# Optimization experiments

Measured on AMD Instinct MI355X. Metric: run time of the kernel, lower is better.

## Reference

```python
import jax, jax.numpy as jnp
import numpy as np

RESO = (128, 128, 128)      # links table resolution
CAP = 1_600_000             # number of occupied voxels (rows in data arrays)
SH_C = 27                   # 3 * basis_dim (basis_dim = 9 SH components)
N_PTS = 2_000_000           # query points (ray samples)
EMPTY_FRAC = 0.24           # fraction of links marked empty (-1)


def setup_inputs() -> dict:
    key = jax.random.key(0)
    k1, k2, k3, k4, k5 = jax.random.split(key, 5)
    density_data = jax.random.normal(k1, (CAP, 1), dtype=jnp.float32)
    sh_data = 0.1 * jax.random.normal(k2, (CAP, SH_C), dtype=jnp.float32)
    links = jax.random.randint(k3, RESO, 0, CAP, dtype=jnp.int32)
    empty = jax.random.uniform(k4, RESO) < EMPTY_FRAC
    links = jnp.where(empty, jnp.int32(-1), links)
    # points in grid coordinates, spanning the full grid
    points = jax.random.uniform(k5, (N_PTS, 3), dtype=jnp.float32,
                                minval=0.0, maxval=float(RESO[0] - 1))
    return {"density_data": density_data, "sh_data": sh_data,
            "links": links, "points": points}


def reference(density_data, sh_data, links, points):
    """Faithful JAX version of _C.sample_grid (want_colors=True):
    trilinear interpolation of sparse voxel data, where voxel -> data-row
    indirection goes through `links` and negative links contribute zero.
    Returns (out_density [N,1], out_sh [N, 27])."""
    reso = jnp.asarray(links.shape, dtype=points.dtype)
    p = jnp.clip(points, 0.0, reso - 1.0)
    l = jnp.clip(jnp.floor(p).astype(jnp.int32), 0,
                 jnp.asarray(links.shape, jnp.int32) - 2)   # [N,3]
    w = p - l.astype(points.dtype)                           # [N,3] in [0,1]

    out_d = jnp.zeros((points.shape[0], density_data.shape[1]), points.dtype)
    out_sh = jnp.zeros((points.shape[0], sh_data.shape[1]), points.dtype)
    # small fixed loop over 8 corners keeps peak memory at O(N * C)
    for dx in (0, 1):
        wx = w[:, 0] if dx else (1.0 - w[:, 0])
        for dy in (0, 1):
            wy = w[:, 1] if dy else (1.0 - w[:, 1])
            for dz in (0, 1):
                wz = w[:, 2] if dz else (1.0 - w[:, 2])
                idx = links[l[:, 0] + dx, l[:, 1] + dy, l[:, 2] + dz]  # [N]
                valid = idx >= 0
                safe = jnp.where(valid, idx, 0)
                wt = (wx * wy * wz * valid.astype(points.dtype))[:, None]
                out_d = out_d + wt * density_data[safe]
                out_sh = out_sh + wt * sh_data[safe]
    return out_d, out_sh
```

## Files before the change

### kernel.cpp

```cpp
#include <hip/hip_runtime.h>
#include <hip/hip_fp16.h>
#include <hip/hip_fp8.h>

#define RESO 128
#define SH_C 27
#define NCELLS (16*16*16)
#define CAPB 608
#define OVF_CAP 16384
#define PACK_ROWS 64
#define PACK_PER_G 16
#define SCAT_PER_G 5
#define GROUP (PACK_PER_G + SCAT_PER_G)
#define OVF_BLOCKS 64
#define NROWS 729
#define QSTEP 1024.0f
#define QINV  (1.0f/1024.0f)

__device__ __forceinline__ void point_to_voxel(float px, float py, float pz,
                                               int& lx, int& ly, int& lz,
                                               float& cx, float& cy, float& cz) {
    cx = fminf(fmaxf(px, 0.0f), (float)(RESO - 1));
    cy = fminf(fmaxf(py, 0.0f), (float)(RESO - 1));
    cz = fminf(fmaxf(pz, 0.0f), (float)(RESO - 1));
    lx = min(max((int)floorf(cx), 0), RESO - 2);
    ly = min(max((int)floorf(cy), 0), RESO - 2);
    lz = min(max((int)floorf(cz), 0), RESO - 2);
}

__device__ __forceinline__ int cell_of(int lx, int ly, int lz) {
    return ((lx >> 3) << 8) | ((ly >> 3) << 4) | (lz >> 3);
}

#if defined(__has_builtin)
#if __has_builtin(__builtin_amdgcn_cvt_pk_f32_fp8)
#define HAVE_CVT_PK_FP8 1
#endif
#endif

typedef float v2f __attribute__((ext_vector_type(2)));

__device__ __forceinline__ float fp8_to_f32_sw(unsigned int b) {
    const unsigned int s = (b >> 7) & 1u, e = (b >> 3) & 15u, m = b & 7u;
    float v;
    if (e == 0) v = (float)m * 0.001953125f;
    else        v = __uint_as_float(((e + 120u) << 23) | (m << 20));
    return s ? -v : v;
}

__device__ __forceinline__ void acc4_fp8(unsigned int w, float wt, float* a) {
#ifdef HAVE_CVT_PK_FP8
    const v2f lo = __builtin_amdgcn_cvt_pk_f32_fp8((int)w, false);
    const v2f hi = __builtin_amdgcn_cvt_pk_f32_fp8((int)w, true);
    a[0] = fmaf(wt, lo.x, a[0]);
    a[1] = fmaf(wt, lo.y, a[1]);
    a[2] = fmaf(wt, hi.x, a[2]);
    a[3] = fmaf(wt, hi.y, a[3]);
#else
    a[0] = fmaf(wt, fp8_to_f32_sw(w & 0xff), a[0]);
    a[1] = fmaf(wt, fp8_to_f32_sw((w >> 8) & 0xff), a[1]);
    a[2] = fmaf(wt, fp8_to_f32_sw((w >> 16) & 0xff), a[2]);
    a[3] = fmaf(wt, fp8_to_f32_sw((w >> 24) & 0xff), a[3]);
#endif
}

__device__ __forceinline__ void accum_row(const uint4& q0, const uint4& q1,
                                          float wt, float& accd, float* accs) {
    accd = fmaf(wt, __uint_as_float(q0.x), accd);
    acc4_fp8(q0.y, wt, accs + 0);
    acc4_fp8(q0.z, wt, accs + 4);
    acc4_fp8(q0.w, wt, accs + 8);
    acc4_fp8(q1.x, wt, accs + 12);
    acc4_fp8(q1.y, wt, accs + 16);
    acc4_fp8(q1.z, wt, accs + 20);
    acc4_fp8(q1.w, wt, accs + 24);
}

__device__ __forceinline__ void write_out(int orig, float accd, const float* accs,
                                          float* __restrict__ out_d,
                                          float* __restrict__ out_sh) {
    out_d[orig] = accd;
    float* __restrict__ o = out_sh + (size_t)orig * SH_C;
    #pragma unroll
    for (int c = 0; c < SH_C; ++c) o[c] = accs[c];
}

__global__ __launch_bounds__(256) void fused_pack_scatter_kernel(
    const float* __restrict__ density, const float* __restrict__ sh,
    uint4* __restrict__ rows, int cap, int gridp,
    const float* __restrict__ pts, int n, int grids,
    int* __restrict__ cnt, int* __restrict__ ovfcnt,
    uint2* __restrict__ bucket, int* __restrict__ ovf)
{
    __shared__ float sv[PACK_ROWS * SH_C];

    const int bid = blockIdx.x;
    const int g = bid / GROUP, rr = bid % GROUP;

    if (rr < PACK_PER_G) {
        const int pid = g * PACK_PER_G + rr;
        if (pid >= gridp) return;
        const int r0 = pid * PACK_ROWS;
        const int nrows = min(PACK_ROWS, cap - r0);
        if (nrows <= 0) return;
        const float* __restrict__ src = sh + (size_t)r0 * SH_C;
        if (nrows == PACK_ROWS) {
            const float4* __restrict__ s4 = (const float4*)src;
            float4* d4 = (float4*)sv;
            for (int k = threadIdx.x; k < PACK_ROWS * SH_C / 4; k += 256) d4[k] = s4[k];
        } else {
            for (int k = threadIdx.x; k < nrows * SH_C; k += 256) sv[k] = src[k];
        }
        __syncthreads();
        const int t   = threadIdx.x;
        const int row = t >> 2;
        const int s   = t & 3;
        if (row < nrows) {
            const int r = r0 + row;
            const float* __restrict__ sr = sv + row * SH_C;
            union { uint2 u; unsigned char b[8]; float f[2]; } pk;
            if (s == 0) {
                pk.f[0] = density[r];
                #pragma unroll
                for (int c = 0; c < 4; ++c)
                    pk.b[4 + c] = __hip_cvt_float_to_fp8(sr[c], __HIP_SATFINITE, __HIP_E4M3);
            } else {
                const int c0 = s * 8 - 4;
                #pragma unroll
                for (int c = 0; c < 8; ++c) {
                    const int cc = c0 + c;
                    pk.b[c] = (cc < SH_C)
                        ? __hip_cvt_float_to_fp8(sr[cc], __HIP_SATFINITE, __HIP_E4M3)
                        : (unsigned char)0;
                }
            }
            *(uint2*)((char*)rows + (size_t)r * 32 + s * 8) = pk.u;
        }
    } else {
        const int sid = g * SCAT_PER_G + (rr - PACK_PER_G);
        if (sid >= grids) return;
        const int i = sid * 256 + threadIdx.x;
        if (i >= n) return;
        const float px = pts[3*(size_t)i], py = pts[3*(size_t)i+1], pz = pts[3*(size_t)i+2];
        int lx, ly, lz; float cx, cy, cz;
        point_to_voxel(px, py, pz, lx, ly, lz, cx, cy, cz);
        const int cell = cell_of(lx, ly, lz);
        const int slot = atomicAdd(&cnt[cell], 1);
        if (slot < CAPB) {
            const unsigned qx = min((unsigned)__float2int_rn((cx - (float)(lx & ~7)) * QSTEP), 8191u);
            const unsigned qy = min((unsigned)__float2int_rn((cy - (float)(ly & ~7)) * QSTEP), 8191u);
            const unsigned qz = min((unsigned)__float2int_rn((cz - (float)(lz & ~7)) * QSTEP), 8191u);
            const unsigned long long v = (unsigned long long)(unsigned)i
                                       | ((unsigned long long)qx << 21)
                                       | ((unsigned long long)qy << 34)
                                       | ((unsigned long long)qz << 47);
            uint2 e; e.x = (unsigned)v; e.y = (unsigned)(v >> 32);
            bucket[(size_t)cell * CAPB + slot] = e;
        } else {
            const int o = atomicAdd(ovfcnt, 1);
            if (o < OVF_CAP) ovf[o] = i;
        }
    }
}

__global__ __launch_bounds__(256) void sample_bucket_kernel(
    const uint4* __restrict__ rows,
    const int*   __restrict__ links,
    const float* __restrict__ pts,
    const uint2* __restrict__ bucket,
    const int*   __restrict__ cnt,
    const int*   __restrict__ ovf,
    const int*   __restrict__ ovfcnt,
    float* __restrict__ out_d,
    float* __restrict__ out_sh)
{
    __shared__ int  slk[NROWS];
    __shared__ uint4 srow[NROWS * 2];

    const int bid = blockIdx.x;
    const int cell = ((bid & 7) << 9) | (bid >> 3);
    const int bx = ((cell >> 8) & 15) << 3;
    const int by = ((cell >> 4) & 15) << 3;
    const int bz = (cell & 15) << 3;
    const int tid = threadIdx.x;

    for (int i = tid; i < NROWS; i += 256) {
        const int rx = i / 81, rem = i - rx * 81;
        const int ry = rem / 9, rz = rem - ry * 9;
        const int gx = min(bx + rx, RESO - 1);
        const int gy = min(by + ry, RESO - 1);
        const int gz = min(bz + rz, RESO - 1);
        slk[i] = links[(gx << 14) | (gy << 7) | gz];
    }
    __syncthreads();

    for (int i = tid; i < NROWS * 2; i += 256) {
        const int lrow = i >> 1, half = i & 1;
        const int link = slk[lrow];
        uint4 v = make_uint4(0u, 0u, 0u, 0u);
        if (link >= 0) v = rows[(size_t)link * 2 + half];
        srow[i] = v;
    }
    __syncthreads();

    const int m = min(cnt[cell], CAPB);

    for (int i = tid; i < m; i += 256) {
        const uint2 e = bucket[(size_t)cell * CAPB + i];
        const unsigned long long v = (unsigned long long)e.x
                                   | ((unsigned long long)e.y << 32);
        const int orig = (int)(v & 0x1FFFFFu);
        const float cx = (float)bx + (float)((v >> 21) & 0x1FFFu) * QINV;
        const float cy = (float)by + (float)((v >> 34) & 0x1FFFu) * QINV;
        const float cz = (float)bz + (float)((v >> 47) & 0x1FFFu) * QINV;

        const int lx = min((int)cx, RESO - 2);
        const int ly = min((int)cy, RESO - 2);
        const int lz = min((int)cz, RESO - 2);

        const float wx = cx - (float)lx;
        const float wy = cy - (float)ly;
        const float wz = cz - (float)lz;
        const int ox = lx - bx, oy = ly - by, oz = lz - bz;

        float accd = 0.0f, accs[28];
        #pragma unroll
        for (int c = 0; c < 28; ++c) accs[c] = 0.0f;

        const int lrow0 = ox * 81 + oy * 9 + oz;
        #pragma unroll
        for (int k = 0; k < 8; ++k) {
            const int dx = (k >> 2) & 1;
            const int dy = (k >> 1) & 1;
            const int dz = k & 1;
            const int lrow = lrow0 + dx * 81 + dy * 9 + dz;
            const float wt = (slk[lrow] >= 0)
                ? (dx ? wx : 1.0f - wx) * (dy ? wy : 1.0f - wy) * (dz ? wz : 1.0f - wz)
                : 0.0f;
            accum_row(srow[lrow * 2], srow[lrow * 2 + 1], wt, accd, accs);
        }

        write_out(orig, accd, accs, out_d, out_sh);
    }

    if (bid < OVF_BLOCKS) {
        const int mo = min(*ovfcnt, OVF_CAP);
        for (int i = bid * 256 + tid; i < mo; i += OVF_BLOCKS * 256) {
            const int orig = ovf[i];
            const float px = pts[3*(size_t)orig];
            const float py = pts[3*(size_t)orig + 1];
            const float pz = pts[3*(size_t)orig + 2];
            int lx, ly, lz; float cx, cy, cz;
            point_to_voxel(px, py, pz, lx, ly, lz, cx, cy, cz);
            const float wx = cx - (float)lx, wy = cy - (float)ly, wz = cz - (float)lz;
            float accd = 0.0f, accs[28];
            #pragma unroll
            for (int c = 0; c < 28; ++c) accs[c] = 0.0f;
            const int base = (lx << 14) + (ly << 7) + lz;
            #pragma unroll
            for (int k = 0; k < 8; ++k) {
                const int dx = (k >> 2) & 1, dy = (k >> 1) & 1, dz = k & 1;
                const int idx = links[base + (dx << 14) + (dy << 7) + dz];
                const int safe = idx < 0 ? 0 : idx;
                const float wt = (idx >= 0)
                    ? (dx ? wx : 1.0f - wx) * (dy ? wy : 1.0f - wy) * (dz ? wz : 1.0f - wz)
                    : 0.0f;
                accum_row(rows[(size_t)safe*2], rows[(size_t)safe*2+1], wt, accd, accs);
            }
            write_out(orig, accd, accs, out_d, out_sh);
        }
    }
}

__global__ __launch_bounds__(256) void sample_direct_kernel(
    const float* __restrict__ density, const float* __restrict__ sh,
    const int* __restrict__ links, const float* __restrict__ points,
    float* __restrict__ out_d, float* __restrict__ out_sh, int n)
{
    int i = blockIdx.x * blockDim.x + threadIdx.x;
    if (i >= n) return;
    int lx, ly, lz; float cx, cy, cz;
    point_to_voxel(points[3*(size_t)i], points[3*(size_t)i+1], points[3*(size_t)i+2],
                   lx, ly, lz, cx, cy, cz);
    const float wx = cx - (float)lx, wy = cy - (float)ly, wz = cz - (float)lz;
    float accd = 0.0f, accs[SH_C];
    #pragma unroll
    for (int c = 0; c < SH_C; ++c) accs[c] = 0.0f;
    const int base = lx * (RESO * RESO) + ly * RESO + lz;
    #pragma unroll
    for (int k = 0; k < 8; ++k) {
        const int dx = (k >> 2) & 1, dy = (k >> 1) & 1, dz = k & 1;
        const int idx = links[base + dx * (RESO * RESO) + dy * RESO + dz];
        if (idx >= 0) {
            const float wt = (dx ? wx : 1.0f - wx) * (dy ? wy : 1.0f - wy) * (dz ? wz : 1.0f - wz);
            accd = fmaf(wt, density[idx], accd);
            const float* row = sh + (size_t)idx * SH_C;
            #pragma unroll
            for (int c = 0; c < SH_C; ++c) accs[c] = fmaf(wt, row[c], accs[c]);
        }
    }
    out_d[i] = accd;
    float* o = out_sh + (size_t)i * SH_C;
    #pragma unroll
    for (int c = 0; c < SH_C; ++c) o[c] = accs[c];
}

extern "C" void kernel_launch(void* const* d_in, const int* in_sizes, int n_in,
                              void* d_out, int out_size, void* d_ws, size_t ws_size,
                              hipStream_t stream) {
    const float* density = (const float*)d_in[0];
    const float* sh      = (const float*)d_in[1];
    const int*   links   = (const int*)d_in[2];
    const float* points  = (const float*)d_in[3];

    const int cap = in_sizes[0];
    const int n   = in_sizes[3] / 3;

    float* out_d  = (float*)d_out;
    float* out_sh = out_d + n;

    const int gridp = (cap + PACK_ROWS - 1) / PACK_ROWS;
    const int grids = (n + 255) / 256;
    const int ngroups = max((gridp + PACK_PER_G - 1) / PACK_PER_G,
                            (grids + SCAT_PER_G - 1) / SCAT_PER_G);

    const size_t cnt_bytes  = (size_t)NCELLS * sizeof(int);
    const size_t ovfc_off   = cnt_bytes;
    const size_t bucket_off = (cnt_bytes + 256 + 255) & ~(size_t)255;
    const size_t ovf_off    = (bucket_off + (size_t)NCELLS * CAPB * sizeof(uint2) + 255) & ~(size_t)255;
    const size_t rows_off   = (ovf_off + (size_t)OVF_CAP * sizeof(int) + 255) & ~(size_t)255;
    const size_t need       = rows_off + (size_t)cap * 32;

    if (ws_size >= need && n < (1 << 21)) {
        int*    cnt    = (int*)d_ws;
        int*    ovfcnt = (int*)((char*)d_ws + ovfc_off);
        uint2*  bucket = (uint2*)((char*)d_ws + bucket_off);
        int*    ovf    = (int*)((char*)d_ws + ovf_off);
        uint4*  rows   = (uint4*)((char*)d_ws + rows_off);

        hipMemsetAsync(d_ws, 0, cnt_bytes + 256, stream);
        fused_pack_scatter_kernel<<<ngroups * GROUP, 256, 0, stream>>>(
            density, sh, rows, cap, gridp, points, n, grids, cnt, ovfcnt, bucket, ovf);
        sample_bucket_kernel<<<NCELLS, 256, 0, stream>>>(rows, links, points, bucket, cnt,
                                                         ovf, ovfcnt, out_d, out_sh);
    } else {
        sample_direct_kernel<<<(n + 255) / 256, 256, 0, stream>>>(
            density, sh, links, points, out_d, out_sh, n);
    }
}
```

Before: 308.1 us.

## Bin points into 4^3 fine cells and gather eight fine buckets per block

Scatter now bins points into 32^3 fine cells with a 96-entry cap instead of 16^3 coarse cells with a 608-entry cap. Each sampling block gathers its eight child fine buckets through a prefix-offset table, and quantization is doubled to 2048 steps. The aim is to spread the atomicAdd counters over many more addresses, cutting contention during scatter, and to make points within a bucket more spatially sorted for better locality. The cost is a larger count memset, a per-point search over the child offsets, and a higher risk of small buckets overflowing into the slower overflow path.

Result: faster. 263.4 us, median of 2 (-14.5%).

```diff
diff --git a/kernel.cpp b/kernel.cpp
--- a/kernel.cpp
+++ b/kernel.cpp
@@ -4,8 +4,9 @@
 
 #define RESO 128
 #define SH_C 27
-#define NCELLS (16*16*16)
-#define CAPB 608
+#define NFINE (32*32*32)
+#define NCOARSE (16*16*16)
+#define CAPB 96
 #define OVF_CAP 16384
 #define PACK_ROWS 64
 #define PACK_PER_G 16
@@ -13,8 +14,8 @@
 #define GROUP (PACK_PER_G + SCAT_PER_G)
 #define OVF_BLOCKS 64
 #define NROWS 729
-#define QSTEP 1024.0f
-#define QINV  (1.0f/1024.0f)
+#define QSTEP 2048.0f
+#define QINV  (1.0f/2048.0f)
 
 __device__ __forceinline__ void point_to_voxel(float px, float py, float pz,
                                                int& lx, int& ly, int& lz,
@@ -27,8 +28,8 @@
     lz = min(max((int)floorf(cz), 0), RESO - 2);
 }
 
-__device__ __forceinline__ int cell_of(int lx, int ly, int lz) {
-    return ((lx >> 3) << 8) | ((ly >> 3) << 4) | (lz >> 3);
+__device__ __forceinline__ int fine_cell_of(int lx, int ly, int lz) {
+    return ((lx >> 2) << 10) | ((ly >> 2) << 5) | (lz >> 2);
 }
 
 #if defined(__has_builtin)
@@ -143,12 +144,12 @@
         const float px = pts[3*(size_t)i], py = pts[3*(size_t)i+1], pz = pts[3*(size_t)i+2];
         int lx, ly, lz; float cx, cy, cz;
         point_to_voxel(px, py, pz, lx, ly, lz, cx, cy, cz);
-        const int cell = cell_of(lx, ly, lz);
+        const int cell = fine_cell_of(lx, ly, lz);
         const int slot = atomicAdd(&cnt[cell], 1);
         if (slot < CAPB) {
-            const unsigned qx = min((unsigned)__float2int_rn((cx - (float)(lx & ~7)) * QSTEP), 8191u);
-            const unsigned qy = min((unsigned)__float2int_rn((cy - (float)(ly & ~7)) * QSTEP), 8191u);
-            const unsigned qz = min((unsigned)__float2int_rn((cz - (float)(lz & ~7)) * QSTEP), 8191u);
+            const unsigned qx = min((unsigned)__float2int_rn((cx - (float)(lx & ~3)) * QSTEP), 8191u);
+            const unsigned qy = min((unsigned)__float2int_rn((cy - (float)(ly & ~3)) * QSTEP), 8191u);
+            const unsigned qz = min((unsigned)__float2int_rn((cz - (float)(lz & ~3)) * QSTEP), 8191u);
             const unsigned long long v = (unsigned long long)(unsigned)i
                                        | ((unsigned long long)qx << 21)
                                        | ((unsigned long long)qy << 34)
@@ -173,8 +174,9 @@
     float* __restrict__ out_d,
     float* __restrict__ out_sh)
 {
-    __shared__ int  slk[NROWS];
+    __shared__ int   slk[NROWS];
     __shared__ uint4 srow[NROWS * 2];
+    __shared__ int   soff[9];
 
     const int bid = blockIdx.x;
     const int cell = ((bid & 7) << 9) | (bid >> 3);
@@ -191,6 +193,19 @@
         const int gz = min(bz + rz, RESO - 1);
         slk[i] = links[(gx << 14) | (gy << 7) | gz];
     }
+    if (tid == 0) {
+        int acc = 0;
+        soff[0] = 0;
+        #pragma unroll
+        for (int f = 0; f < 8; ++f) {
+            const int fx = (bx >> 2) + ((f >> 2) & 1);
+            const int fy = (by >> 2) + ((f >> 1) & 1);
+            const int fz = (bz >> 2) + (f & 1);
+            const int fc = (fx << 10) | (fy << 5) | fz;
+            acc += min(cnt[fc], CAPB);
+            soff[f + 1] = acc;
+        }
+    }
     __syncthreads();
 
     for (int i = tid; i < NROWS * 2; i += 256) {
@@ -202,16 +217,24 @@
     }
     __syncthreads();
 
-    const int m = min(cnt[cell], CAPB);
-
-    for (int i = tid; i < m; i += 256) {
-        const uint2 e = bucket[(size_t)cell * CAPB + i];
+    const int M = soff[8];
+
+    for (int j = tid; j < M; j += 256) {
+        int f = 0;
+        #pragma unroll
+        for (int t = 1; t < 8; ++t) f += (j >= soff[t]);
+        const int fx = (bx >> 2) + ((f >> 2) & 1);
+        const int fy = (by >> 2) + ((f >> 1) & 1);
+        const int fz = (bz >> 2) + (f & 1);
+        const int fc = (fx << 10) | (fy << 5) | fz;
+
+        const uint2 e = bucket[(size_t)fc * CAPB + (j - soff[f])];
         const unsigned long long v = (unsigned long long)e.x
                                    | ((unsigned long long)e.y << 32);
         const int orig = (int)(v & 0x1FFFFFu);
-        const float cx = (float)bx + (float)((v >> 21) & 0x1FFFu) * QINV;
-        const float cy = (float)by + (float)((v >> 34) & 0x1FFFu) * QINV;
-        const float cz = (float)bz + (float)((v >> 47) & 0x1FFFu) * QINV;
+        const float cx = (float)(fx << 2) + (float)((v >> 21) & 0x1FFFu) * QINV;
+        const float cy = (float)(fy << 2) + (float)((v >> 34) & 0x1FFFu) * QINV;
+        const float cz = (float)(fz << 2) + (float)((v >> 47) & 0x1FFFu) * QINV;
 
         const int lx = min((int)cx, RESO - 2);
         const int ly = min((int)cy, RESO - 2);
@@ -323,10 +346,10 @@
     const int ngroups = max((gridp + PACK_PER_G - 1) / PACK_PER_G,
                             (grids + SCAT_PER_G - 1) / SCAT_PER_G);
 
-    const size_t cnt_bytes  = (size_t)NCELLS * sizeof(int);
+    const size_t cnt_bytes  = (size_t)NFINE * sizeof(int);
     const size_t ovfc_off   = cnt_bytes;
     const size_t bucket_off = (cnt_bytes + 256 + 255) & ~(size_t)255;
-    const size_t ovf_off    = (bucket_off + (size_t)NCELLS * CAPB * sizeof(uint2) + 255) & ~(size_t)255;
+    const size_t ovf_off    = (bucket_off + (size_t)NFINE * CAPB * sizeof(uint2) + 255) & ~(size_t)255;
     const size_t rows_off   = (ovf_off + (size_t)OVF_CAP * sizeof(int) + 255) & ~(size_t)255;
     const size_t need       = rows_off + (size_t)cap * 32;
 
@@ -340,8 +363,8 @@
         hipMemsetAsync(d_ws, 0, cnt_bytes + 256, stream);
         fused_pack_scatter_kernel<<<ngroups * GROUP, 256, 0, stream>>>(
             density, sh, rows, cap, gridp, points, n, grids, cnt, ovfcnt, bucket, ovf);
-        sample_bucket_kernel<<<NCELLS, 256, 0, stream>>>(rows, links, points, bucket, cnt,
-                                                         ovf, ovfcnt, out_d, out_sh);
+        sample_bucket_kernel<<<NCOARSE, 256, 0, stream>>>(rows, links, points, bucket, cnt,
+                                                          ovf, ovfcnt, out_d, out_sh);
     } else {
         sample_direct_kernel<<<(n + 255) / 256, 256, 0, stream>>>(
             density, sh, links, points, out_d, out_sh, n);
```
